# Performance work log

Measured on AMD Instinct MI355X. Metric: run time of the kernel, lower is better.

Reference implementation:

```python
import jax, jax.numpy as jnp
import numpy as np

B, S, C, MID = 32, 8192, 256, 128

def setup_inputs() -> dict:
    key = jax.random.key(0)
    k_x, k_w1, k_b1, k_w2, k_b2 = jax.random.split(key, 5)
    bound1 = 1.0 / np.sqrt(C)
    bound2 = 1.0 / np.sqrt(MID)
    return {
        "x": jax.random.normal(k_x, (B, S, C), dtype=jnp.float32),
        "W1": jax.random.uniform(k_w1, (C, MID), jnp.float32, -bound1, bound1),
        "b1": jax.random.uniform(k_b1, (MID,), jnp.float32, -bound1, bound1),
        "w2": jax.random.uniform(k_w2, (MID,), jnp.float32, -bound2, bound2),
        "b2": jax.random.uniform(k_b2, (), jnp.float32, -bound2, bound2),
    }

def reference(x, W1, b1, w2, b2):
    # scores: (B, S) — dropout is identity in eval mode
    h = jnp.tanh(jnp.einsum("bsc,cm->bsm", x, W1) + b1)       # (B, S, MID)
    scores = jnp.einsum("bsm,m->bs", h, w2) + b2              # (B, S)
    attn = jax.nn.softmax(scores, axis=-1)                    # softmax over seq
    out = jnp.einsum("bsc,bs->bc", x, attn)                   # weighted sum over seq
    return out
```

## Files before the change

### kernel.cpp

```cpp
#include <hip/hip_runtime.h>
#include <hip/hip_bf16.h>


typedef __attribute__((ext_vector_type(8))) short short8;
typedef __attribute__((ext_vector_type(4))) float f32x4;
typedef unsigned short u16;

constexpr int Bb = 32;
constexpr int Ss = 8192;
constexpr int Cc = 256;
constexpr int MIDm = 128;
constexpr int BM = 128;
constexpr int NBLK = Bb * Ss / BM;
constexpr int BPB = Ss / BM;

__device__ __forceinline__ u16 f2bf(float f) {
  return __builtin_bit_cast(u16, __float2bfloat16(f));
}

__global__ __launch_bounds__(256) void wprep_kernel(
    const float* __restrict__ W1, u16* __restrict__ FB)
{
  const int t    = blockIdx.x * 256 + threadIdx.x;
  const int lane = t & 63;
  const int nt   = (t >> 6) & 1;
  const int kcc  = (t >> 7) & 7;
  const int wc   = (t >> 10) & 3;
  const int n    = wc * 32 + nt * 16 + (lane & 15);
  const int k0   = kcc * 32 + (lane >> 4) * 8;
  union { u16 v[8]; short8 s; } u;
  #pragma unroll
  for (int e = 0; e < 8; ++e) u.v[e] = f2bf(W1[(size_t)(k0 + e) * MIDm + n]);
  *(short8*)(FB + (size_t)t * 8) = u.s;
}

__global__ __launch_bounds__(256, 2) void fused_kernel(
    const float* __restrict__ x, const u16* __restrict__ FB,
    const float* __restrict__ b1, const float* __restrict__ w2,
    float* __restrict__ oPart, float* __restrict__ mPart, float* __restrict__ lPart)
{
  __shared__ __align__(16) char smem[65536];
  const int tid  = threadIdx.x;
  const int lane = tid & 63;
  const int w    = tid >> 6;
  const int q    = lane >> 4;
  const int ln   = lane & 15;
  const int row0 = blockIdx.x * BM;

  short8 Bf[8][2];
  {
    const u16* fbw = FB + ((size_t)(w * 8) * 2 + 0) * 64 * 8;
    #pragma unroll
    for (int kcc = 0; kcc < 8; ++kcc)
      #pragma unroll
      for (int nt = 0; nt < 2; ++nt)
        Bf[kcc][nt] = *(const short8*)(FB +
            ((size_t)(((w * 8 + kcc) * 2 + nt) * 64 + lane)) * 8);
    (void)fbw;
  }

  f32x4 acc[4][2][2];
  #pragma unroll
  for (int nt = 0; nt < 2; ++nt) {
    float bj = b1[32 * w + 16 * nt + ln];
    #pragma unroll
    for (int sl = 0; sl < 4; ++sl)
      #pragma unroll
      for (int mt = 0; mt < 2; ++mt) {
        acc[sl][mt][nt][0] = bj; acc[sl][mt][nt][1] = bj;
        acc[sl][mt][nt][2] = bj; acc[sl][mt][nt][3] = bj;
      }
  }

  #define STAGE(buf, sl)                                                              \
    {                                                                                 \
      _Pragma("unroll")                                                               \
      for (int r = 0; r < 8; ++r) {                                                   \
        int L     = r * 4096 + tid * 16;                                              \
        int row   = L >> 10;                                                          \
        int inrow = (L & 1023) ^ ((row & 7) << 4);                                    \
        const char* src = (const char*)x                                              \
            + (size_t)(row0 + (sl) * 32 + row) * 1024 + inrow;                        \
        __builtin_amdgcn_global_load_lds(                                             \
            (const __attribute__((address_space(1))) void*)src,                       \
            (__attribute__((address_space(3))) void*)(smem + (buf) * 32768 + L),      \
            16, 0, 0);                                                                \
      }                                                                               \
    }

  STAGE(0, 0);

  #pragma unroll
  for (int sl = 0; sl < 4; ++sl) {
    const int cur = sl & 1;
    if (sl < 3) STAGE(1 - cur, sl + 1);

    __builtin_amdgcn_sched_barrier(0);
    if (sl < 3) asm volatile("s_waitcnt vmcnt(8)" ::: "memory");
    else        asm volatile("s_waitcnt vmcnt(0)" ::: "memory");
    __builtin_amdgcn_sched_barrier(0);
    __builtin_amdgcn_s_barrier();
    __builtin_amdgcn_sched_barrier(0);

    const char* bufb = smem + cur * 32768;
    #pragma unroll
    for (int kcc = 0; kcc < 8; ++kcc) {
      #pragma unroll
      for (int mt = 0; mt < 2; ++mt) {
        const int row = 16 * mt + ln;
        const int sw  = (row & 7) << 4;
        const char* base = bufb + row * 1024;
        const int off = kcc * 128 + q * 32;
        float4 lo = *(const float4*)(base + (off ^ sw));
        float4 hi = *(const float4*)(base + ((off + 16) ^ sw));
        union { u16 v[8]; short8 s8; } t8;
        t8.v[0] = f2bf(lo.x); t8.v[1] = f2bf(lo.y); t8.v[2] = f2bf(lo.z); t8.v[3] = f2bf(lo.w);
        t8.v[4] = f2bf(hi.x); t8.v[5] = f2bf(hi.y); t8.v[6] = f2bf(hi.z); t8.v[7] = f2bf(hi.w);
        #pragma unroll
        for (int nt = 0; nt < 2; ++nt)
          acc[sl][mt][nt] = __builtin_amdgcn_mfma_f32_16x16x32_bf16(
              t8.s8, Bf[kcc][nt], acc[sl][mt][nt], 0, 0, 0);
      }
    }

    __builtin_amdgcn_sched_barrier(0);
    __builtin_amdgcn_s_barrier();
  }

  float* sScore = (float*)smem;
  float* sP     = (float*)(smem + 2048);
  float* sO     = (float*)(smem + 2560);
  float* sML    = (float*)(smem + 6656);

  float w2v[2];
  #pragma unroll
  for (int nt = 0; nt < 2; ++nt) w2v[nt] = w2[32 * w + 16 * nt + ln];

  #pragma unroll
  for (int sl = 0; sl < 4; ++sl)
    #pragma unroll
    for (int mt = 0; mt < 2; ++mt) {
      float p[4];
      #pragma unroll
      for (int r = 0; r < 4; ++r) p[r] = 0.f;
      #pragma unroll
      for (int nt = 0; nt < 2; ++nt)
        #pragma unroll
        for (int r = 0; r < 4; ++r)
          p[r] += (1.0f - 2.0f / (__expf(2.0f * acc[sl][mt][nt][r]) + 1.0f)) * w2v[nt];
      #pragma unroll
      for (int off = 1; off < 16; off <<= 1)
        #pragma unroll
        for (int r = 0; r < 4; ++r) p[r] += __shfl_xor(p[r], off);
      if (ln == 0) {
        #pragma unroll
        for (int r = 0; r < 4; ++r)
          sScore[w * BM + 32 * sl + 16 * mt + 4 * q + r] = p[r];
      }
    }
  __syncthreads();

  if (tid < BM)
    sP[tid] = sScore[tid] + sScore[BM + tid] + sScore[2 * BM + tid] + sScore[3 * BM + tid];
  __syncthreads();
  if (w == 0) {
    float a = sP[lane], b = sP[lane + 64];
    float m = fmaxf(a, b);
    #pragma unroll
    for (int off = 1; off < 64; off <<= 1) m = fmaxf(m, __shfl_xor(m, off));
    float e0 = __expf(a - m), e1 = __expf(b - m);
    sP[lane] = e0; sP[lane + 64] = e1;
    float s = e0 + e1;
    #pragma unroll
    for (int off = 1; off < 64; off <<= 1) s += __shfl_xor(s, off);
    if (lane == 0) { sML[0] = m; sML[1] = s; }
  }
  __syncthreads();

  const int c4 = tid & 63;
  const int rg = tid >> 6;
  const float* xo = x + (size_t)(row0 + rg * 32) * Cc + c4 * 4;
  float4 o = make_float4(0.f, 0.f, 0.f, 0.f);
  #pragma unroll 8
  for (int r = 0; r < 32; ++r) {
    float pw = sP[rg * 32 + r];
    float4 xv = *(const float4*)(xo + (size_t)r * Cc);
    o.x = fmaf(pw, xv.x, o.x);
    o.y = fmaf(pw, xv.y, o.y);
    o.z = fmaf(pw, xv.z, o.z);
    o.w = fmaf(pw, xv.w, o.w);
  }
  *(float4*)&sO[rg * Cc + c4 * 4] = o;
  __syncthreads();

  float oc = sO[tid] + sO[Cc + tid] + sO[2 * Cc + tid] + sO[3 * Cc + tid];
  oPart[(size_t)blockIdx.x * Cc + tid] = oc;
  if (tid == 0) { mPart[blockIdx.x] = sML[0]; lPart[blockIdx.x] = sML[1]; }
}

__global__ __launch_bounds__(256) void combine_kernel(
    const float* __restrict__ oPart, const float* __restrict__ mPart,
    const float* __restrict__ lPart, float* __restrict__ out)
{
  const int b = blockIdx.x;
  const int t = threadIdx.x;
  float M = -3.4e38f;
  for (int k = 0; k < BPB; ++k) M = fmaxf(M, mPart[b * BPB + k]);
  float num = 0.f, den = 0.f;
  for (int k = 0; k < BPB; ++k) {
    float wgt = __expf(mPart[b * BPB + k] - M);
    den += wgt * lPart[b * BPB + k];
    num = fmaf(wgt, oPart[(size_t)(b * BPB + k) * Cc + t], num);
  }
  out[b * Cc + t] = num / den;
}

extern "C" void kernel_launch(void* const* d_in, const int* in_sizes, int n_in,
                              void* d_out, int out_size, void* d_ws, size_t ws_size,
                              hipStream_t stream)
{
  const float* x  = (const float*)d_in[0];
  const float* W1 = (const float*)d_in[1];
  const float* b1 = (const float*)d_in[2];
  const float* w2 = (const float*)d_in[3];
  float* out = (float*)d_out;

  u16*   FB    = (u16*)d_ws;
  float* oPart = (float*)((char*)d_ws + 65536);
  float* mPart = (float*)((char*)d_ws + 65536 + 2097152);
  float* lPart = (float*)((char*)d_ws + 65536 + 2097152 + 8192);

  wprep_kernel<<<16, 256, 0, stream>>>(W1, FB);
  fused_kernel<<<NBLK, 256, 0, stream>>>(x, FB, b1, w2, oPart, mPart, lPart);
  combine_kernel<<<Bb, Cc, 0, stream>>>(oPart, mPart, lPart, out);
}
```

Before: 102.3 us.

## Shrink blocks to 32 rows, split MID fully per wave, reuse LDS x tile

Each block now handles 32 rows with 2 waves. Each wave loads its own 16-row x tile to LDS once and computes all 128 hidden units, streaming W1 fragments from global memory with double buffering instead of holding them in registers. The weighted-sum pass reads x from the LDS tile instead of re-reading it from global memory, which removes the second pass over x. The trade-off is four times more blocks and partials, so the combine kernel reads more data, W1 fragments are reloaded for every tile, and there is no prefetch overlap across tiles within a block.

```diff
diff --git a/kernel.cpp b/kernel.cpp
--- a/kernel.cpp
+++ b/kernel.cpp
@@ -10,7 +10,7 @@
 constexpr int Ss = 8192;
 constexpr int Cc = 256;
 constexpr int MIDm = 128;
-constexpr int BM = 128;
+constexpr int BM = 32;
 constexpr int NBLK = Bb * Ss / BM;
 constexpr int BPB = Ss / BM;
 
@@ -23,178 +23,143 @@
 {
   const int t    = blockIdx.x * 256 + threadIdx.x;
   const int lane = t & 63;
-  const int nt   = (t >> 6) & 1;
-  const int kcc  = (t >> 7) & 7;
-  const int wc   = (t >> 10) & 3;
-  const int n    = wc * 32 + nt * 16 + (lane & 15);
-  const int k0   = kcc * 32 + (lane >> 4) * 8;
+  const int nt   = (t >> 6) & 7;
+  const int kc   = (t >> 9) & 7;
+  const int n    = nt * 16 + (lane & 15);
+  const int k0   = kc * 32 + (lane >> 4) * 8;
   union { u16 v[8]; short8 s; } u;
   #pragma unroll
   for (int e = 0; e < 8; ++e) u.v[e] = f2bf(W1[(size_t)(k0 + e) * MIDm + n]);
   *(short8*)(FB + (size_t)t * 8) = u.s;
 }
 
-__global__ __launch_bounds__(256, 2) void fused_kernel(
+__global__ __launch_bounds__(128, 2) void fused_kernel(
     const float* __restrict__ x, const u16* __restrict__ FB,
     const float* __restrict__ b1, const float* __restrict__ w2,
     float* __restrict__ oPart, float* __restrict__ mPart, float* __restrict__ lPart)
 {
-  __shared__ __align__(16) char smem[65536];
+  __shared__ __align__(16) char tile[2 * 16 * 1024];
+  __shared__ float sScore[BM];
+  __shared__ float sP[BM];
+  __shared__ float sO[2][Cc];
+  __shared__ float sML[2];
+
   const int tid  = threadIdx.x;
   const int lane = tid & 63;
   const int w    = tid >> 6;
   const int q    = lane >> 4;
   const int ln   = lane & 15;
   const int row0 = blockIdx.x * BM;
-
-  short8 Bf[8][2];
+  const int wrow0 = row0 + w * 16;
+
+  char* ldsw = tile + w * 16384;
+
   {
-    const u16* fbw = FB + ((size_t)(w * 8) * 2 + 0) * 64 * 8;
-    #pragma unroll
-    for (int kcc = 0; kcc < 8; ++kcc)
-      #pragma unroll
-      for (int nt = 0; nt < 2; ++nt)
-        Bf[kcc][nt] = *(const short8*)(FB +
-            ((size_t)(((w * 8 + kcc) * 2 + nt) * 64 + lane)) * 8);
-    (void)fbw;
-  }
-
-  f32x4 acc[4][2][2];
-  #pragma unroll
-  for (int nt = 0; nt < 2; ++nt) {
-    float bj = b1[32 * w + 16 * nt + ln];
-    #pragma unroll
-    for (int sl = 0; sl < 4; ++sl)
-      #pragma unroll
-      for (int mt = 0; mt < 2; ++mt) {
-        acc[sl][mt][nt][0] = bj; acc[sl][mt][nt][1] = bj;
-        acc[sl][mt][nt][2] = bj; acc[sl][mt][nt][3] = bj;
-      }
-  }
-
-  #define STAGE(buf, sl)                                                              \
-    {                                                                                 \
-      _Pragma("unroll")                                                               \
-      for (int r = 0; r < 8; ++r) {                                                   \
-        int L     = r * 4096 + tid * 16;                                              \
-        int row   = L >> 10;                                                          \
-        int inrow = (L & 1023) ^ ((row & 7) << 4);                                    \
-        const char* src = (const char*)x                                              \
-            + (size_t)(row0 + (sl) * 32 + row) * 1024 + inrow;                        \
-        __builtin_amdgcn_global_load_lds(                                             \
-            (const __attribute__((address_space(1))) void*)src,                       \
-            (__attribute__((address_space(3))) void*)(smem + (buf) * 32768 + L),      \
-            16, 0, 0);                                                                \
-      }                                                                               \
+    const char* xb = (const char*)x + (size_t)wrow0 * 1024;
+    #pragma unroll
+    for (int i = 0; i < 16; ++i) {
+      const char* src = xb + (size_t)i * 1024 + ((lane * 16) ^ ((i & 7) << 4));
+      __builtin_amdgcn_global_load_lds(
+          (const __attribute__((address_space(1))) void*)src,
+          (__attribute__((address_space(3))) void*)(ldsw + i * 1024),
+          16, 0, 0);
     }
-
-  STAGE(0, 0);
-
-  #pragma unroll
-  for (int sl = 0; sl < 4; ++sl) {
-    const int cur = sl & 1;
-    if (sl < 3) STAGE(1 - cur, sl + 1);
-
-    __builtin_amdgcn_sched_barrier(0);
-    if (sl < 3) asm volatile("s_waitcnt vmcnt(8)" ::: "memory");
-    else        asm volatile("s_waitcnt vmcnt(0)" ::: "memory");
-    __builtin_amdgcn_sched_barrier(0);
-    __builtin_amdgcn_s_barrier();
-    __builtin_amdgcn_sched_barrier(0);
-
-    const char* bufb = smem + cur * 32768;
-    #pragma unroll
-    for (int kcc = 0; kcc < 8; ++kcc) {
-      #pragma unroll
-      for (int mt = 0; mt < 2; ++mt) {
-        const int row = 16 * mt + ln;
-        const int sw  = (row & 7) << 4;
-        const char* base = bufb + row * 1024;
-        const int off = kcc * 128 + q * 32;
-        float4 lo = *(const float4*)(base + (off ^ sw));
-        float4 hi = *(const float4*)(base + ((off + 16) ^ sw));
-        union { u16 v[8]; short8 s8; } t8;
-        t8.v[0] = f2bf(lo.x); t8.v[1] = f2bf(lo.y); t8.v[2] = f2bf(lo.z); t8.v[3] = f2bf(lo.w);
-        t8.v[4] = f2bf(hi.x); t8.v[5] = f2bf(hi.y); t8.v[6] = f2bf(hi.z); t8.v[7] = f2bf(hi.w);
-        #pragma unroll
-        for (int nt = 0; nt < 2; ++nt)
-          acc[sl][mt][nt] = __builtin_amdgcn_mfma_f32_16x16x32_bf16(
-              t8.s8, Bf[kcc][nt], acc[sl][mt][nt], 0, 0, 0);
-      }
-    }
-
-    __builtin_amdgcn_sched_barrier(0);
-    __builtin_amdgcn_s_barrier();
-  }
-
-  float* sScore = (float*)smem;
-  float* sP     = (float*)(smem + 2048);
-  float* sO     = (float*)(smem + 2560);
-  float* sML    = (float*)(smem + 6656);
-
-  float w2v[2];
-  #pragma unroll
-  for (int nt = 0; nt < 2; ++nt) w2v[nt] = w2[32 * w + 16 * nt + ln];
-
-  #pragma unroll
-  for (int sl = 0; sl < 4; ++sl)
-    #pragma unroll
-    for (int mt = 0; mt < 2; ++mt) {
-      float p[4];
-      #pragma unroll
-      for (int r = 0; r < 4; ++r) p[r] = 0.f;
-      #pragma unroll
-      for (int nt = 0; nt < 2; ++nt)
-        #pragma unroll
-        for (int r = 0; r < 4; ++r)
-          p[r] += (1.0f - 2.0f / (__expf(2.0f * acc[sl][mt][nt][r]) + 1.0f)) * w2v[nt];
-      #pragma unroll
-      for (int off = 1; off < 16; off <<= 1)
-        #pragma unroll
-        for (int r = 0; r < 4; ++r) p[r] += __shfl_xor(p[r], off);
-      if (ln == 0) {
-        #pragma unroll
-        for (int r = 0; r < 4; ++r)
-          sScore[w * BM + 32 * sl + 16 * mt + 4 * q + r] = p[r];
-      }
-    }
+  }
+
+  f32x4 acc[8];
+  #pragma unroll
+  for (int nt = 0; nt < 8; ++nt) {
+    float bj = b1[nt * 16 + ln];
+    acc[nt][0] = bj; acc[nt][1] = bj; acc[nt][2] = bj; acc[nt][3] = bj;
+  }
+
+  short8 Bf[2][8];
+  #define LDB(ph, kc_)                                                        \
+    { _Pragma("unroll")                                                       \
+      for (int nt = 0; nt < 8; ++nt)                                          \
+        Bf[ph][nt] = *(const short8*)(FB + ((size_t)((kc_) * 8 + nt) * 64 + lane) * 8); }
+
+  LDB(0, 0)
+
+  __builtin_amdgcn_sched_barrier(0);
+  asm volatile("s_waitcnt vmcnt(0)" ::: "memory");
+  __builtin_amdgcn_sched_barrier(0);
+
+  const int sw = (ln & 7) << 4;
+  const char* abase = ldsw + ln * 1024;
+
+  #pragma unroll
+  for (int kc = 0; kc < 8; ++kc) {
+    const int ph = kc & 1;
+    if (kc < 7) LDB(1 - ph, kc + 1)
+    const int off = kc * 128 + q * 32;
+    float4 lo = *(const float4*)(abase + (off ^ sw));
+    float4 hi = *(const float4*)(abase + ((off + 16) ^ sw));
+    union { u16 v[8]; short8 s8; } t8;
+    t8.v[0] = f2bf(lo.x); t8.v[1] = f2bf(lo.y); t8.v[2] = f2bf(lo.z); t8.v[3] = f2bf(lo.w);
+    t8.v[4] = f2bf(hi.x); t8.v[5] = f2bf(hi.y); t8.v[6] = f2bf(hi.z); t8.v[7] = f2bf(hi.w);
+    #pragma unroll
+    for (int nt = 0; nt < 8; ++nt)
+      acc[nt] = __builtin_amdgcn_mfma_f32_16x16x32_bf16(t8.s8, Bf[ph][nt], acc[nt], 0, 0, 0);
+  }
+
+  float w2v[8];
+  #pragma unroll
+  for (int nt = 0; nt < 8; ++nt) w2v[nt] = w2[nt * 16 + ln];
+
+  float p[4] = {0.f, 0.f, 0.f, 0.f};
+  #pragma unroll
+  for (int nt = 0; nt < 8; ++nt)
+    #pragma unroll
+    for (int r = 0; r < 4; ++r)
+      p[r] += (1.0f - 2.0f / (__expf(2.0f * acc[nt][r]) + 1.0f)) * w2v[nt];
+
+  #pragma unroll
+  for (int off = 1; off < 16; off <<= 1)
+    #pragma unroll
+    for (int r = 0; r < 4; ++r) p[r] += __shfl_xor(p[r], off);
+
+  if (ln == 0) {
+    #pragma unroll
+    for (int r = 0; r < 4; ++r) sScore[w * 16 + q * 4 + r] = p[r];
+  }
   __syncthreads();
 
-  if (tid < BM)
-    sP[tid] = sScore[tid] + sScore[BM + tid] + sScore[2 * BM + tid] + sScore[3 * BM + tid];
+  if (w == 0) {
+    float v = (lane < BM) ? sScore[lane] : -3.4e38f;
+    float m = v;
+    #pragma unroll
+    for (int off = 1; off < 64; off <<= 1) m = fmaxf(m, __shfl_xor(m, off));
+    float e = (lane < BM) ? __expf(v - m) : 0.f;
+    float s = e;
+    #pragma unroll
+    for (int off = 1; off < 64; off <<= 1) s += __shfl_xor(s, off);
+    if (lane < BM) sP[lane] = e;
+    if (lane == 0) { sML[0] = m; sML[1] = s; }
+  }
   __syncthreads();
-  if (w == 0) {
-    float a = sP[lane], b = sP[lane + 64];
-    float m = fmaxf(a, b);
-    #pragma unroll
-    for (int off = 1; off < 64; off <<= 1) m = fmaxf(m, __shfl_xor(m, off));
-    float e0 = __expf(a - m), e1 = __expf(b - m);
-    sP[lane] = e0; sP[lane + 64] = e1;
-    float s = e0 + e1;
-    #pragma unroll
-    for (int off = 1; off < 64; off <<= 1) s += __shfl_xor(s, off);
-    if (lane == 0) { sML[0] = m; sML[1] = s; }
-  }
-  __syncthreads();
-
-  const int c4 = tid & 63;
-  const int rg = tid >> 6;
-  const float* xo = x + (size_t)(row0 + rg * 32) * Cc + c4 * 4;
+
   float4 o = make_float4(0.f, 0.f, 0.f, 0.f);
-  #pragma unroll 8
-  for (int r = 0; r < 32; ++r) {
-    float pw = sP[rg * 32 + r];
-    float4 xv = *(const float4*)(xo + (size_t)r * Cc);
+  #pragma unroll
+  for (int i = 0; i < 16; ++i) {
+    float pw = sP[w * 16 + i];
+    float4 xv = *(const float4*)(ldsw + i * 1024 + ((lane * 16) ^ ((i & 7) << 4)));
     o.x = fmaf(pw, xv.x, o.x);
     o.y = fmaf(pw, xv.y, o.y);
     o.z = fmaf(pw, xv.z, o.z);
     o.w = fmaf(pw, xv.w, o.w);
   }
-  *(float4*)&sO[rg * Cc + c4 * 4] = o;
+  *(float4*)&sO[w][lane * 4] = o;
   __syncthreads();
 
-  float oc = sO[tid] + sO[Cc + tid] + sO[2 * Cc + tid] + sO[3 * Cc + tid];
-  oPart[(size_t)blockIdx.x * Cc + tid] = oc;
+  {
+    const int c0 = tid, c1 = tid + 128;
+    float a0 = sO[0][c0] + sO[1][c0];
+    float a1 = sO[0][c1] + sO[1][c1];
+    float* op = oPart + (size_t)blockIdx.x * Cc;
+    op[c0] = a0;
+    op[c1] = a1;
+  }
   if (tid == 0) { mPart[blockIdx.x] = sML[0]; lPart[blockIdx.x] = sML[1]; }
 }
 
@@ -227,10 +192,10 @@
 
   u16*   FB    = (u16*)d_ws;
   float* oPart = (float*)((char*)d_ws + 65536);
-  float* mPart = (float*)((char*)d_ws + 65536 + 2097152);
-  float* lPart = (float*)((char*)d_ws + 65536 + 2097152 + 8192);
+  float* mPart = (float*)((char*)d_ws + 65536 + 8388608);
+  float* lPart = (float*)((char*)d_ws + 65536 + 8388608 + 32768);
 
   wprep_kernel<<<16, 256, 0, stream>>>(W1, FB);
-  fused_kernel<<<NBLK, 256, 0, stream>>>(x, FB, b1, w2, oPart, mPart, lPart);
+  fused_kernel<<<NBLK, 128, 0, stream>>>(x, FB, b1, w2, oPart, mPart, lPart);
   combine_kernel<<<Bb, Cc, 0, stream>>>(oPart, mPart, lPart, out);
 }
```

Result: slower. 112.1 us (+9.6%).
